# Optimization experiments

Measured on AMD Instinct MI355X. Metric: run time of the kernel, lower is better.

## Reference

```python
import jax, jax.numpy as jnp
import numpy as np

HEADS = 8
DIM_HEAD = 32
TOP_K = 256
KMEANS_ITERS = 10
EPS_LN = 1e-6
EPS_L2 = 1e-12


def chan_layer_norm(x, gamma, beta):
    # x: (b, c, L); normalize across channel dim (biased variance)
    mean = jnp.mean(x, axis=1, keepdims=True)
    var = jnp.var(x, axis=1, keepdims=True)
    return gamma * (x - mean) / (jnp.sqrt(var) + EPS_LN) + beta


def l2norm_ch(t):
    # F.normalize(t, dim=1): L2-normalize over channel axis of (B, c, L)
    n = jnp.linalg.norm(t, axis=1, keepdims=True)
    return t / jnp.maximum(n, EPS_L2)


def conv1x1(x, w):
    # x: (b, c_in, L), w: (c_out, c_in)  -> (b, c_out, L)
    return jnp.einsum('oc,bcl->bol', w, x)


def _dist2(x, c):
    # squared L2 distances, x: (N, d), c: (k, d) -> (N, k)
    return (jnp.sum(x * x, -1, keepdims=True)
            - 2.0 * x @ c.T
            + jnp.sum(c * c, -1)[None, :])


def kmeans_fit(x, k, iters):
    # Lloyd's algorithm, deterministic init = first k points
    c0 = x[:k]

    def step(c, _):
        assign = jnp.argmin(_dist2(x, c), axis=-1)           # (N,)
        sums = jax.ops.segment_sum(x, assign, num_segments=k)
        cnts = jax.ops.segment_sum(jnp.ones((x.shape[0],), x.dtype), assign,
                                   num_segments=k)
        new_c = jnp.where(cnts[:, None] > 0,
                          sums / jnp.maximum(cnts, 1.0)[:, None], c)
        return new_c, None

    c, _ = jax.lax.scan(step, c0, None, length=iters)
    return c


def select_best_ind(q, k, v, top_k):
    # q: (B, Lq, d), k/v: (B, Lk, d); B = b*heads
    B, Lk, d = k.shape
    q_flat = q.reshape(-1, d)
    centroids = kmeans_fit(q_flat, top_k, KMEANS_ITERS)       # (top_k, d)
    k_flat = k.reshape(-1, d)
    k_cluster = jnp.argmin(_dist2(k_flat, centroids), axis=-1).reshape(B, Lk)
    k_centers = centroids[k_cluster]                          # (B, Lk, d)
    k_dist = jnp.sum(jnp.abs(k_centers - k), axis=-1)         # (B, Lk)
    _, best_k = jax.lax.top_k(k_dist, top_k)                  # largest dists
    idx = best_k[:, :, None]
    k_sel = jnp.take_along_axis(k, idx, axis=1)
    v_sel = jnp.take_along_axis(v, idx, axis=1)
    return k_sel, v_sel


def reference(query_source, context, w_q, w_kv, w_out,
              ln_ctx_gamma, ln_ctx_beta, ln_q_gamma, ln_q_beta,
              ln_out_gamma, ln_out_beta, gamma_scale):
    b, c, L_query = query_source.shape
    ctx = chan_layer_norm(context, ln_ctx_gamma, ln_ctx_beta)
    qs = chan_layer_norm(query_source, ln_q_gamma, ln_q_beta)

    kv = conv1x1(ctx, w_kv)                                   # (b, 2*inner, Lc)
    k, v = jnp.split(kv, 2, axis=1)
    q = conv1x1(qs, w_q)                                      # (b, inner, Lq)

    def fold(t):  # b (h c) L -> (b h) c L
        B, hc, L = t.shape
        return t.reshape(B, HEADS, DIM_HEAD, L).reshape(B * HEADS, DIM_HEAD, L)

    q, k, v = fold(q), fold(k), fold(v)
    q, k = l2norm_ch(q), l2norm_ch(k)
    # b d L -> b L d
    q = jnp.swapaxes(q, 1, 2)
    k = jnp.swapaxes(k, 1, 2)
    v = jnp.swapaxes(v, 1, 2)

    k, v = select_best_ind(q, k, v, TOP_K)

    sim = jnp.einsum('bid,bjd->bij', q, k)                    # (b*h, Lq, top_k)
    attn = jax.nn.softmax(sim, axis=-1)
    out = jnp.einsum('bij,bjd->bid', attn, v)                 # (b*h, Lq, dh)

    out = out.reshape(b, HEADS, L_query, DIM_HEAD)
    out = jnp.transpose(out, (0, 1, 3, 2)).reshape(b, HEADS * DIM_HEAD, L_query)
    out = conv1x1(out, w_out)
    out = chan_layer_norm(out, ln_out_gamma, ln_out_beta)
    return gamma_scale[0] * out + query_source


def setup_inputs() -> dict:
    key = jax.random.key(0)
    ks = jax.random.split(key, 8)
    dim, inner = 256, HEADS * DIM_HEAD
    b, Lq, Lc = 2, 4096, 4096
    inp = {
        'query_source': jax.random.normal(ks[0], (b, dim, Lq), jnp.float32),
        'context': jax.random.normal(ks[1], (b, dim, Lc), jnp.float32),
        'w_q': jax.random.normal(ks[2], (inner, dim), jnp.float32) * 0.05,
        'w_kv': jax.random.normal(ks[3], (2 * inner, dim), jnp.float32) * 0.05,
        'w_out': jax.random.normal(ks[4], (dim, inner), jnp.float32) * 0.05,
        'ln_ctx_gamma': jnp.ones((1, dim, 1), jnp.float32),
        'ln_ctx_beta': jnp.zeros((1, dim, 1), jnp.float32),
        'ln_q_gamma': jnp.ones((1, dim, 1), jnp.float32),
        'ln_q_beta': jnp.zeros((1, dim, 1), jnp.float32),
        'ln_out_gamma': jnp.ones((1, dim, 1), jnp.float32),
        'ln_out_beta': jnp.zeros((1, dim, 1), jnp.float32),
        'gamma_scale': jax.random.normal(ks[5], (1,), jnp.float32),
    }
    return inp
```

## Files before the change

### kernel.cpp

```cpp
#include <hip/hip_runtime.h>
#include <math.h>

#define CDIM 256
#define LSEQ 4096
#define NBH 16
#define NPTS 65536
#define KC 256

__device__ __forceinline__ float fadd(float a, float b){ return __fadd_rn(a,b); }
__device__ __forceinline__ float fmul(float a, float b){ return __fmul_rn(a,b); }
__device__ __forceinline__ float fsub(float a, float b){ return __fsub_rn(a,b); }

__device__ __forceinline__ void gld_lds4(const float* g, float* l){
    __builtin_amdgcn_global_load_lds(
        (const __attribute__((address_space(1))) unsigned int*)g,
        (__attribute__((address_space(3))) unsigned int*)l, 4, 0, 0);
}

__device__ __forceinline__ float sum32_np(const float* e){
    float l[16];
    #pragma unroll
    for (int j = 0; j < 16; j++) l[j] = fadd(e[j], e[j + 16]);
    float t3[8];
    #pragma unroll
    for (int j = 0; j < 8; j++) t3[j] = fadd(l[j], l[j + 8]);
    float t6[4];
    #pragma unroll
    for (int j = 0; j < 4; j++) t6[j] = fadd(t3[j], t3[j + 4]);
    return fadd(fadd(t6[0], t6[2]), fadd(t6[1], t6[3]));
}

__global__ __launch_bounds__(64) void ln2_np(
        const float* __restrict__ x0, const float* __restrict__ g0,
        const float* __restrict__ bt0, float* __restrict__ y0,
        const float* __restrict__ x1, const float* __restrict__ g1,
        const float* __restrict__ bt1, float* __restrict__ y1) {
    __shared__ float xl[256 * 64];
    int tid = threadIdx.x;
    int gid = blockIdx.x * 64 + tid;
    int which = gid >> 13;
    int r = gid & 8191;
    int b = r >> 12, l = r & 4095;
    const float* x  = which ? x1 : x0;
    const float* g  = which ? g1 : g0;
    const float* bt = which ? bt1 : bt0;
    float* y        = which ? y1 : y0;
    const float* xb = x + (size_t)b * CDIM * LSEQ + l;
    #pragma unroll 8
    for (int c = 0; c < 256; c++)
        gld_lds4(xb + (size_t)c * LSEQ, xl + c * 64);
    __syncthreads();
    float s = 0.f;
    #pragma unroll 8
    for (int c = 0; c < 256; c++) s = fadd(s, xl[c * 64 + tid]);
    float mean = __fdiv_rn(s, 256.f);
    float s2 = 0.f;
    #pragma unroll 8
    for (int c = 0; c < 256; c++) {
        float d = fsub(xl[c * 64 + tid], mean);
        s2 = fadd(s2, fmul(d, d));
    }
    float var = __fdiv_rn(s2, 256.f);
    float den = fadd(__fsqrt_rn(var), 1e-6f);
    float* yb = y + (size_t)b * CDIM * LSEQ + l;
    #pragma unroll 4
    for (int c = 0; c < 256; c++) {
        float d = fsub(xl[c * 64 + tid], mean);
        yb[(size_t)c * LSEQ] = fadd(__fdiv_rn(fmul(g[c], d), den), bt[c]);
    }
}

__global__ __launch_bounds__(256) void conv_all16(
        const float* __restrict__ Wkv, const float* __restrict__ Xkv,
        float* __restrict__ Ykv,
        const float* __restrict__ Wq, const float* __restrict__ Xq,
        float* __restrict__ Yq) {
    int tid = threadIdx.x;
    int l0 = blockIdx.x * 512 + tid * 2;
    bool qpath = blockIdx.y >= 32;
    int yb = qpath ? (blockIdx.y - 32) : blockIdx.y;
    int o0 = yb * 16;
    int b = blockIdx.z;
    const float4* w4 = (const float4*)((qpath ? Wq : Wkv) + (size_t)o0 * CDIM);
    const float* X = qpath ? Xq : Xkv;
    const float* xb = X + (size_t)b * CDIM * LSEQ;
    float acc[16][2];
    #pragma unroll
    for (int oo = 0; oo < 16; oo++) { acc[oo][0] = 0.f; acc[oo][1] = 0.f; }
    bool sop = qpath || (blockIdx.y < 16);
    if (sop) {
        for (int c = 0; c < 256; c += 4) {
            float2 x0q = *(const float2*)(xb + (size_t)(c + 0) * LSEQ + l0);
            float2 x1q = *(const float2*)(xb + (size_t)(c + 1) * LSEQ + l0);
            float2 x2q = *(const float2*)(xb + (size_t)(c + 2) * LSEQ + l0);
            float2 x3q = *(const float2*)(xb + (size_t)(c + 3) * LSEQ + l0);
            #pragma unroll
            for (int oo = 0; oo < 16; oo++) {
                float4 w = w4[(oo * 256 + c) >> 2];
                acc[oo][0] = fadd(acc[oo][0], fmul(w.x, x0q.x));
                acc[oo][0] = fadd(acc[oo][0], fmul(w.y, x1q.x));
                acc[oo][0] = fadd(acc[oo][0], fmul(w.z, x2q.x));
                acc[oo][0] = fadd(acc[oo][0], fmul(w.w, x3q.x));
                acc[oo][1] = fadd(acc[oo][1], fmul(w.x, x0q.y));
                acc[oo][1] = fadd(acc[oo][1], fmul(w.y, x1q.y));
                acc[oo][1] = fadd(acc[oo][1], fmul(w.z, x2q.y));
                acc[oo][1] = fadd(acc[oo][1], fmul(w.w, x3q.y));
            }
        }
    } else {
        for (int c = 0; c < 256; c += 4) {
            float2 x0q = *(const float2*)(xb + (size_t)(c + 0) * LSEQ + l0);
            float2 x1q = *(const float2*)(xb + (size_t)(c + 1) * LSEQ + l0);
            float2 x2q = *(const float2*)(xb + (size_t)(c + 2) * LSEQ + l0);
            float2 x3q = *(const float2*)(xb + (size_t)(c + 3) * LSEQ + l0);
            #pragma unroll
            for (int oo = 0; oo < 16; oo++) {
                float4 w = w4[(oo * 256 + c) >> 2];
                acc[oo][0] = __builtin_fmaf(w.x, x0q.x, acc[oo][0]);
                acc[oo][0] = __builtin_fmaf(w.y, x1q.x, acc[oo][0]);
                acc[oo][0] = __builtin_fmaf(w.z, x2q.x, acc[oo][0]);
                acc[oo][0] = __builtin_fmaf(w.w, x3q.x, acc[oo][0]);
                acc[oo][1] = __builtin_fmaf(w.x, x0q.y, acc[oo][1]);
                acc[oo][1] = __builtin_fmaf(w.y, x1q.y, acc[oo][1]);
                acc[oo][1] = __builtin_fmaf(w.z, x2q.y, acc[oo][1]);
                acc[oo][1] = __builtin_fmaf(w.w, x3q.y, acc[oo][1]);
            }
        }
    }
    float* Y = qpath ? Yq : Ykv;
    int rows = qpath ? 256 : 512;
    #pragma unroll
    for (int oo = 0; oo < 16; oo++)
        *(float2*)(Y + ((size_t)b * rows + o0 + oo) * LSEQ + l0) =
            make_float2(acc[oo][0], acc[oo][1]);
}

template<bool EXACT>
__global__ __launch_bounds__(256) void conv_q8(const float* __restrict__ W,
        const float* __restrict__ X, float* __restrict__ Y) {
    __shared__ float ws[8 * 256];
    int tid = threadIdx.x;
    int l0 = blockIdx.x * 1024 + tid * 4;
    int o0 = blockIdx.y * 8;
    int b = blockIdx.z;
    {
        const float4* wb4 = (const float4*)(W + (size_t)o0 * CDIM);
        float4* ws4s = (float4*)ws;
        for (int i = tid; i < 8 * 64; i += 256) ws4s[i] = wb4[i];
    }
    __syncthreads();
    const float* xb = X + (size_t)b * CDIM * LSEQ;
    float acc[8][4];
    #pragma unroll
    for (int oo = 0; oo < 8; oo++)
        #pragma unroll
        for (int i = 0; i < 4; i++) acc[oo][i] = 0.f;
    const float4* ws4 = (const float4*)ws;
    for (int c = 0; c < 256; c += 4) {
        float4 x0q = *(const float4*)(xb + (size_t)(c + 0) * LSEQ + l0);
        float4 x1q = *(const float4*)(xb + (size_t)(c + 1) * LSEQ + l0);
        float4 x2q = *(const float4*)(xb + (size_t)(c + 2) * LSEQ + l0);
        float4 x3q = *(const float4*)(xb + (size_t)(c + 3) * LSEQ + l0);
        #pragma unroll
        for (int oo = 0; oo < 8; oo++) {
            float4 w = ws4[(oo * 256 + c) >> 2];
            if (EXACT) {
                acc[oo][0] = fadd(acc[oo][0], fmul(w.x, x0q.x));
                acc[oo][0] = fadd(acc[oo][0], fmul(w.y, x1q.x));
                acc[oo][0] = fadd(acc[oo][0], fmul(w.z, x2q.x));
                acc[oo][0] = fadd(acc[oo][0], fmul(w.w, x3q.x));
                acc[oo][1] = fadd(acc[oo][1], fmul(w.x, x0q.y));
                acc[oo][1] = fadd(acc[oo][1], fmul(w.y, x1q.y));
                acc[oo][1] = fadd(acc[oo][1], fmul(w.z, x2q.y));
                acc[oo][1] = fadd(acc[oo][1], fmul(w.w, x3q.y));
                acc[oo][2] = fadd(acc[oo][2], fmul(w.x, x0q.z));
                acc[oo][2] = fadd(acc[oo][2], fmul(w.y, x1q.z));
                acc[oo][2] = fadd(acc[oo][2], fmul(w.z, x2q.z));
                acc[oo][2] = fadd(acc[oo][2], fmul(w.w, x3q.z));
                acc[oo][3] = fadd(acc[oo][3], fmul(w.x, x0q.w));
                acc[oo][3] = fadd(acc[oo][3], fmul(w.y, x1q.w));
                acc[oo][3] = fadd(acc[oo][3], fmul(w.z, x2q.w));
                acc[oo][3] = fadd(acc[oo][3], fmul(w.w, x3q.w));
            } else {
                acc[oo][0] = __builtin_fmaf(w.x, x0q.x, acc[oo][0]);
                acc[oo][0] = __builtin_fmaf(w.y, x1q.x, acc[oo][0]);
                acc[oo][0] = __builtin_fmaf(w.z, x2q.x, acc[oo][0]);
                acc[oo][0] = __builtin_fmaf(w.w, x3q.x, acc[oo][0]);
                acc[oo][1] = __builtin_fmaf(w.x, x0q.y, acc[oo][1]);
                acc[oo][1] = __builtin_fmaf(w.y, x1q.y, acc[oo][1]);
                acc[oo][1] = __builtin_fmaf(w.z, x2q.y, acc[oo][1]);
                acc[oo][1] = __builtin_fmaf(w.w, x3q.y, acc[oo][1]);
                acc[oo][2] = __builtin_fmaf(w.x, x0q.z, acc[oo][2]);
                acc[oo][2] = __builtin_fmaf(w.y, x1q.z, acc[oo][2]);
                acc[oo][2] = __builtin_fmaf(w.z, x2q.z, acc[oo][2]);
                acc[oo][2] = __builtin_fmaf(w.w, x3q.z, acc[oo][2]);
                acc[oo][3] = __builtin_fmaf(w.x, x0q.w, acc[oo][3]);
                acc[oo][3] = __builtin_fmaf(w.y, x1q.w, acc[oo][3]);
                acc[oo][3] = __builtin_fmaf(w.z, x2q.w, acc[oo][3]);
                acc[oo][3] = __builtin_fmaf(w.w, x3q.w, acc[oo][3]);
            }
        }
    }
    #pragma unroll
    for (int oo = 0; oo < 8; oo++)
        *(float4*)(Y + ((size_t)b * 256 + o0 + oo) * LSEQ + l0) =
            make_float4(acc[oo][0], acc[oo][1], acc[oo][2], acc[oo][3]);
}

__device__ __forceinline__ void fold_body(const float* __restrict__ src,
        int srcRows, int row0, int donorm, float* __restrict__ dst,
        float* __restrict__ xxout, float* __restrict__ centout,
        float* __restrict__ ccout, int p) {
    int bh = p >> 12, l = p & 4095;
    int b = bh >> 3, h = bh & 7;
    const float* sp = src + ((size_t)b * srcRows + row0 + h * 32) * LSEQ + l;
    float x[32];
    #pragma unroll
    for (int t = 0; t < 32; t++) x[t] = sp[(size_t)t * LSEQ];
    float4* dp4 = (float4*)(dst + (size_t)p * 32);
    if (donorm) {
        float ss = 0.f;
        #pragma unroll
        for (int t = 0; t < 32; t++) ss = fadd(ss, fmul(x[t], x[t]));
        float n = __fsqrt_rn(ss);
        float den = fmaxf(n, 1e-12f);
        #pragma unroll
        for (int t = 0; t < 32; t++) x[t] = __fdiv_rn(x[t], den);
    }
    #pragma unroll
    for (int t = 0; t < 8; t++)
        dp4[t] = make_float4(x[4*t], x[4*t+1], x[4*t+2], x[4*t+3]);
    if (xxout) {
        float e[32];
        #pragma unroll
        for (int t = 0; t < 32; t++) e[t] = fmul(x[t], x[t]);
        float xv = sum32_np(e);
        xxout[p] = xv;
        if (centout && p < KC) {
            float4* cp4 = (float4*)(centout + (size_t)p * 32);
            #pragma unroll
            for (int t = 0; t < 8; t++)
                cp4[t] = make_float4(x[4*t], x[4*t+1], x[4*t+2], x[4*t+3]);
            ccout[p] = xv;
        }
    }
}

__global__ __launch_bounds__(256) void fold3_np(const float* __restrict__ kvbuf,
        const float* __restrict__ qbuf, float* __restrict__ k_t,
        float* __restrict__ v_t, float* __restrict__ q_t,
        float* __restrict__ xx, float* __restrict__ cent, float* __restrict__ cc) {
    int blk = blockIdx.x, tid = threadIdx.x;
    if (blk < 256) {
        fold_body(kvbuf, 512, 0, 1, k_t, nullptr, nullptr, nullptr, blk * 256 + tid);
    } else if (blk < 512) {
        fold_body(kvbuf, 512, 256, 0, v_t, nullptr, nullptr, nullptr, (blk - 256) * 256 + tid);
    } else {
        fold_body(qbuf, 256, 0, 1, q_t, xx, cent, cc, (blk - 512) * 256 + tid);
    }
}

__global__ __launch_bounds__(256) void assign_h(const float* __restrict__ pts,
        const float* __restrict__ xx, const float* __restrict__ cent,
        const float* __restrict__ cc, float* __restrict__ bdg, int* __restrict__ bjg) {
    __shared__ float sc[128 * 36];
    __shared__ float scc[128];
    int tid = threadIdx.x;
    int c = blockIdx.x >> 1, h = blockIdx.x & 1;
    {
        const float4* c4 = (const float4*)(cent + (size_t)h * 128 * 32);
        for (int i = tid; i < 128 * 8; i += 256) {
            int row = i >> 3, t = i & 7;
            ((float4*)(sc + row * 36))[t] = c4[i];
        }
    }
    if (tid < 128) scc[tid] = cc[h * 128 + tid];
    __syncthreads();
    int pg = tid >> 2, quarter = tid & 3;
    int pb = c * 256 + pg * 4;
    float x[4][32];
    float xp[4];
    #pragma unroll
    for (int i = 0; i < 4; i++) {
        const float4* pp = (const float4*)(pts + (size_t)(pb + i) * 32);
        #pragma unroll
        for (int t = 0; t < 8; t++) {
            float4 f = pp[t];
            x[i][4*t] = f.x; x[i][4*t+1] = f.y; x[i][4*t+2] = f.z; x[i][4*t+3] = f.w;
        }
        xp[i] = xx[pb + i];
    }
    float bd[4] = {3.4e38f, 3.4e38f, 3.4e38f, 3.4e38f};
    int bj[4] = {0x7fffffff, 0x7fffffff, 0x7fffffff, 0x7fffffff};
    for (int jj = 0; jj < 32; jj++) {
        int j = (jj << 2) | quarter;
        const float4* cj = (const float4*)(sc + j * 36);
        float w[32];
        #pragma unroll
        for (int t = 0; t < 8; t++) {
            float4 f = cj[t];
            w[4*t] = f.x; w[4*t+1] = f.y; w[4*t+2] = f.z; w[4*t+3] = f.w;
        }
        float sj = scc[j];
        int jg = h * 128 + j;
        #pragma unroll
        for (int i = 0; i < 4; i++) {
            float g = 0.f;
            #pragma unroll
            for (int t = 0; t < 32; t++) g = __builtin_fmaf(x[i][t], w[t], g);
            float d = fadd(fsub(xp[i], fmul(2.f, g)), sj);
            if (d < bd[i]) { bd[i] = d; bj[i] = jg; }
        }
    }
    #pragma unroll
    for (int i = 0; i < 4; i++) {
        float ob; int oj;
        ob = __shfl_xor(bd[i], 1); oj = __shfl_xor(bj[i], 1);
        if (ob < bd[i] || (ob == bd[i] && oj < bj[i])) { bd[i] = ob; bj[i] = oj; }
        ob = __shfl_xor(bd[i], 2); oj = __shfl_xor(bj[i], 2);
        if (ob < bd[i] || (ob == bd[i] && oj < bj[i])) { bd[i] = ob; bj[i] = oj; }
    }
    if (quarter == 0) {
        #pragma unroll
        for (int i = 0; i < 4; i++) {
            bdg[(size_t)h * NPTS + pb + i] = bd[i];
            bjg[(size_t)h * NPTS + pb + i] = bj[i];
        }
    }
}

__global__ __launch_bounds__(256) void merge_asn(const float* __restrict__ bdg,
        const int* __restrict__ bjg, int* __restrict__ asn, int* __restrict__ hist) {
    __shared__ int bins[256];
    int tid = threadIdx.x, c = blockIdx.x;
    bins[tid] = 0;
    __syncthreads();
    int p = c * 256 + tid;
    float d0 = bdg[p], d1 = bdg[NPTS + p];
    int j = (d1 < d0) ? bjg[NPTS + p] : bjg[p];
    asn[p] = j;
    atomicAdd(&bins[j], 1);
    __syncthreads();
    hist[c * 256 + tid] = bins[tid];
}

__global__ __launch_bounds__(256) void scan_chunks(const int* __restrict__ hist,
        int* __restrict__ chunkbase, int* __restrict__ totals) {
    __shared__ int a[256];
    int j = blockIdx.x, c = threadIdx.x;
    a[c] = hist[(size_t)c * 256 + j];
    __syncthreads();
    for (int d = 1; d < 256; d <<= 1) {
        int v = a[c];
        int u = (c >= d) ? a[c - d] : 0;
        __syncthreads();
        a[c] = v + u;
        __syncthreads();
    }
    chunkbase[(size_t)c * 256 + j] = (c == 0) ? 0 : a[c - 1];
    if (c == 255) totals[j] = a[255];
}

__global__ __launch_bounds__(256) void scatter_v5(const int* __restrict__ asn,
        const int* __restrict__ chunkbase, const int* __restrict__ totals,
        int* __restrict__ perm) {
    __shared__ int cb[256];
    __shared__ int al[256];
    int c = blockIdx.x, tid = threadIdx.x;
    cb[tid] = totals[tid];
    al[tid] = asn[c * 256 + tid];
    __syncthreads();
    for (int d = 1; d < 256; d <<= 1) {
        int v = cb[tid];
        int u = (tid >= d) ? cb[tid - d] : 0;
        __syncthreads();
        cb[tid] = v + u;
        __syncthreads();
    }
    int my = al[tid];
    int base = (my == 0) ? 0 : cb[my - 1];
    int r = 0;
    for (int i = 0; i < tid; i++) r += (al[i] == my) ? 1 : 0;
    perm[base + chunkbase[(size_t)c * 256 + my] + r] = c * 256 + tid;
}

#define STILE 128
__global__ __launch_bounds__(256) void sumk_v4(const float* __restrict__ pts,
        const int* __restrict__ perm, const int* __restrict__ totals,
        float* __restrict__ cent, float* __restrict__ cc) {
    __shared__ int cb[256];
    __shared__ float buf[2][STILE][32];
    int j = blockIdx.x, tid = threadIdx.x;
    cb[tid] = totals[tid];
    __syncthreads();
    for (int d = 1; d < 256; d <<= 1) {
        int v = cb[tid];
        int u = (tid >= d) ? cb[tid - d] : 0;
        __syncthreads();
        cb[tid] = v + u;
        __syncthreads();
    }
    int base = (j == 0) ? 0 : cb[j - 1];
    int n = totals[j];
    int t = tid & 31, r0 = tid >> 5;
    for (int r = r0; r < STILE; r += 8) {
        if (r < n) buf[0][r][t] = pts[(size_t)perm[base + r] * 32 + t];
    }
    __syncthreads();
    float s = 0.f;
    int b = 0;
    for (int i0 = 0; i0 < n; i0 += STILE, b ^= 1) {
        int nx = i0 + STILE;
        if (nx < n) {
            for (int r = r0; r < STILE; r += 8) {
                int g = nx + r;
                if (g < n) buf[b ^ 1][r][t] = pts[(size_t)perm[base + g] * 32 + t];
            }
        }
        if (tid < 32) {
            int m = n - i0; if (m > STILE) m = STILE;
            int i = 0;
            for (; i + 4 <= m; i += 4) {
                s = fadd(s, buf[b][i][tid]);
                s = fadd(s, buf[b][i + 1][tid]);
                s = fadd(s, buf[b][i + 2][tid]);
                s = fadd(s, buf[b][i + 3][tid]);
            }
            for (; i < m; i++) s = fadd(s, buf[b][i][tid]);
        }
        __syncthreads();
    }
    if (tid < 32) {
        float v;
        if (n > 0) {
            v = __fdiv_rn(s, (float)n);
            cent[(size_t)j * 32 + tid] = v;
        } else {
            v = cent[(size_t)j * 32 + tid];
        }
        float e = fmul(v, v);
        e = fadd(e, __shfl_xor(e, 16));
        e = fadd(e, __shfl_xor(e, 8));
        e = fadd(e, __shfl_xor(e, 4));
        e = fadd(e, __shfl_xor(e, 2));
        e = fadd(e, __shfl_xor(e, 1));
        if (tid == 0) cc[j] = e;
    }
}

__global__ __launch_bounds__(256) void kdist4p(const float* __restrict__ pts,
        const float* __restrict__ cent, const float* __restrict__ cc,
        float* __restrict__ kd) {
    __shared__ float sc[256 * 36];
    __shared__ float scc[256];
    int tid = threadIdx.x, c = blockIdx.x;
    {
        const float4* c4 = (const float4*)cent;
        for (int i = tid; i < 256 * 8; i += 256) {
            int row = i >> 3, t = i & 7;
            ((float4*)(sc + row * 36))[t] = c4[i];
        }
    }
    scc[tid] = cc[tid];
    __syncthreads();
    int pg = tid >> 2, quarter = tid & 3;
    int pb = c * 256 + pg * 4;
    float x[4][32];
    float xp[4];
    #pragma unroll
    for (int i = 0; i < 4; i++) {
        const float4* pp = (const float4*)(pts + (size_t)(pb + i) * 32);
        #pragma unroll
        for (int t = 0; t < 8; t++) {
            float4 f = pp[t];
            x[i][4*t] = f.x; x[i][4*t+1] = f.y; x[i][4*t+2] = f.z; x[i][4*t+3] = f.w;
        }
        float e[32];
        #pragma unroll
        for (int t = 0; t < 32; t++) e[t] = fmul(x[i][t], x[i][t]);
        xp[i] = sum32_np(e);
    }
    float bd[4] = {3.4e38f, 3.4e38f, 3.4e38f, 3.4e38f};
    int bj[4] = {0x7fffffff, 0x7fffffff, 0x7fffffff, 0x7fffffff};
    for (int jj = 0; jj < 64; jj++) {
        int j = (jj << 2) | quarter;
        const float4* cj = (const float4*)(sc + j * 36);
        float w[32];
        #pragma unroll
        for (int t = 0; t < 8; t++) {
            float4 f = cj[t];
            w[4*t] = f.x; w[4*t+1] = f.y; w[4*t+2] = f.z; w[4*t+3] = f.w;
        }
        float sj = scc[j];
        #pragma unroll
        for (int i = 0; i < 4; i++) {
            float g = 0.f;
            #pragma unroll
            for (int t = 0; t < 32; t++) g = __builtin_fmaf(x[i][t], w[t], g);
            float d = fadd(fsub(xp[i], fmul(2.f, g)), sj);
            if (d < bd[i]) { bd[i] = d; bj[i] = j; }
        }
    }
    #pragma unroll
    for (int i = 0; i < 4; i++) {
        float ob; int oj;
        ob = __shfl_xor(bd[i], 1); oj = __shfl_xor(bj[i], 1);
        if (ob < bd[i] || (ob == bd[i] && oj < bj[i])) { bd[i] = ob; bj[i] = oj; }
        ob = __shfl_xor(bd[i], 2); oj = __shfl_xor(bj[i], 2);
        if (ob < bd[i] || (ob == bd[i] && oj < bj[i])) { bd[i] = ob; bj[i] = oj; }
    }
    if (quarter == 0) {
        #pragma unroll
        for (int i = 0; i < 4; i++) {
            const float* cb = &sc[bj[i] * 36];
            float e[32];
            #pragma unroll
            for (int t = 0; t < 32; t++) e[t] = fabsf(fsub(cb[t], x[i][t]));
            kd[pb + i] = sum32_np(e);
        }
    }
}

__global__ __launch_bounds__(256) void topk_v3(const float* __restrict__ kd,
        const float* __restrict__ k_t, const float* __restrict__ v_t,
        float* __restrict__ ksel, float* __restrict__ vsel) {
    __shared__ int wsum[4];
    __shared__ int sc1[256];
    __shared__ int out_src[256];
    int bh = blockIdx.x, tid = threadIdx.x;
    int wave = tid >> 6, lane = tid & 63;
    unsigned uv[16];
    {
        const unsigned* kdu = (const unsigned*)(kd + (size_t)bh * 4096);
        #pragma unroll
        for (int q = 0; q < 16; q++) uv[q] = kdu[tid * 16 + q];
    }
    unsigned T = 0u;
    for (int bit = 31; bit >= 0; bit--) {
        unsigned cand = T | (1u << bit);
        int c = 0;
        #pragma unroll
        for (int q = 0; q < 16; q++) c += (uv[q] >= cand) ? 1 : 0;
        c += __shfl_xor(c, 32); c += __shfl_xor(c, 16); c += __shfl_xor(c, 8);
        c += __shfl_xor(c, 4);  c += __shfl_xor(c, 2);  c += __shfl_xor(c, 1);
        if (lane == 0) wsum[wave] = c;
        __syncthreads();
        int tot = wsum[0] + wsum[1] + wsum[2] + wsum[3];
        __syncthreads();
        if (tot >= 256) T = cand;
    }
    int r;
    {
        int c = 0;
        #pragma unroll
        for (int q = 0; q < 16; q++) c += (uv[q] > T) ? 1 : 0;
        c += __shfl_xor(c, 32); c += __shfl_xor(c, 16); c += __shfl_xor(c, 8);
        c += __shfl_xor(c, 4);  c += __shfl_xor(c, 2);  c += __shfl_xor(c, 1);
        if (lane == 0) wsum[wave] = c;
        __syncthreads();
        r = 256 - (wsum[0] + wsum[1] + wsum[2] + wsum[3]);
        __syncthreads();
    }
    int ec = 0;
    #pragma unroll
    for (int q = 0; q < 16; q++) ec += (uv[q] == T) ? 1 : 0;
    sc1[tid] = ec;
    __syncthreads();
    for (int d = 1; d < 256; d <<= 1) {
        int t0 = sc1[tid];
        int u0 = (tid >= d) ? sc1[tid - d] : 0;
        __syncthreads();
        sc1[tid] = t0 + u0;
        __syncthreads();
    }
    int erank = (tid == 0) ? 0 : sc1[tid - 1];
    __syncthreads();
    bool incl[16];
    int ic = 0;
    #pragma unroll
    for (int q = 0; q < 16; q++) {
        unsigned u = uv[q];
        bool inc;
        if (u > T) inc = true;
        else if (u == T) { inc = (erank < r); erank++; }
        else inc = false;
        incl[q] = inc;
        ic += inc ? 1 : 0;
    }
    sc1[tid] = ic;
    __syncthreads();
    for (int d = 1; d < 256; d <<= 1) {
        int t0 = sc1[tid];
        int u0 = (tid >= d) ? sc1[tid - d] : 0;
        __syncthreads();
        sc1[tid] = t0 + u0;
        __syncthreads();
    }
    int pos = (tid == 0) ? 0 : sc1[tid - 1];
    int base_i = tid * 16;
    #pragma unroll
    for (int q = 0; q < 16; q++) {
        if (incl[q]) out_src[pos++] = base_i + q;
    }
    __syncthreads();
    for (int e = tid; e < 256 * 32; e += 256) {
        int jj = e >> 5, t = e & 31;
        int src = out_src[jj];
        ksel[(size_t)bh * 8192 + e] = k_t[((size_t)bh * 4096 + src) * 32 + t];
        vsel[(size_t)bh * 8192 + e] = v_t[((size_t)bh * 4096 + src) * 32 + t];
    }
}

#define HP4 2052
__global__ __launch_bounds__(256, 2) void attn_v4(const float* __restrict__ q_t,
        const float* __restrict__ ksel, const float* __restrict__ vsel,
        float* __restrict__ out) {
    __shared__ float sk[4 * HP4];
    __shared__ float sv[4 * HP4];
    int bh = blockIdx.y, tid = threadIdx.x;
    {
        const float4* gk = (const float4*)(ksel + (size_t)bh * 8192);
        const float4* gv = (const float4*)(vsel + (size_t)bh * 8192);
        for (int i = tid; i < 2048; i += 256) {
            int s = i >> 9, idx = i & 511;
            ((float4*)(sk + s * HP4))[idx] = gk[i];
            ((float4*)(sv + s * HP4))[idx] = gv[i];
        }
    }
    __syncthreads();
    int grp = tid >> 3;
    int dh = tid & 1;
    int slice = (tid >> 1) & 3;
    int p0 = bh * 4096 + blockIdx.x * 128 + grp * 4;
    float q[4][16];
    #pragma unroll
    for (int i = 0; i < 4; i++) {
        const float4* qp = (const float4*)(q_t + (size_t)(p0 + i) * 32 + dh * 16);
        #pragma unroll
        for (int t = 0; t < 4; t++) {
            float4 f = qp[t];
            q[i][4*t] = f.x; q[i][4*t+1] = f.y; q[i][4*t+2] = f.z; q[i][4*t+3] = f.w;
        }
    }
    float o[4][16];
    #pragma unroll
    for (int i = 0; i < 4; i++)
        #pragma unroll
        for (int t = 0; t < 16; t++) o[i][t] = 0.f;
    float ls[4] = {0.f, 0.f, 0.f, 0.f};
    const float* kb = sk + slice * HP4 + dh * 16;
    const float* vb = sv + slice * HP4 + dh * 16;
    for (int j = 0; j < 64; j++) {
        float kf[16];
        #pragma unroll
        for (int t = 0; t < 4; t++) {
            float4 f = *(const float4*)(kb + j * 32 + t * 4);
            kf[4*t] = f.x; kf[4*t+1] = f.y; kf[4*t+2] = f.z; kf[4*t+3] = f.w;
        }
        float ps[4];
        #pragma unroll
        for (int i = 0; i < 4; i++) {
            float a = 0.f, b2 = 0.f, c2 = 0.f, d2 = 0.f;
            #pragma unroll
            for (int t = 0; t < 4; t++) {
                a  += q[i][4*t]   * kf[4*t];
                b2 += q[i][4*t+1] * kf[4*t+1];
                c2 += q[i][4*t+2] * kf[4*t+2];
                d2 += q[i][4*t+3] * kf[4*t+3];
            }
            ps[i] = (a + b2) + (c2 + d2);
        }
        #pragma unroll
        for (int i = 0; i < 4; i++) ps[i] += __shfl_xor(ps[i], 1);
        float w[4];
        #pragma unroll
        for (int i = 0; i < 4; i++) {
            w[i] = __expf(ps[i] - 1.0f);
            ls[i] += w[i];
        }
        float vf[16];
        #pragma unroll
        for (int t = 0; t < 4; t++) {
            float4 f = *(const float4*)(vb + j * 32 + t * 4);
            vf[4*t] = f.x; vf[4*t+1] = f.y; vf[4*t+2] = f.z; vf[4*t+3] = f.w;
        }
        #pragma unroll
        for (int i = 0; i < 4; i++)
            #pragma unroll
            for (int t = 0; t < 16; t++) o[i][t] += w[i] * vf[t];
    }
    #pragma unroll
    for (int i = 0; i < 4; i++) {
        #pragma unroll
        for (int t = 0; t < 16; t++) {
            o[i][t] += __shfl_xor(o[i][t], 2);
            o[i][t] += __shfl_xor(o[i][t], 4);
        }
        ls[i] += __shfl_xor(ls[i], 2);
        ls[i] += __shfl_xor(ls[i], 4);
    }
    if (slice == 0) {
        #pragma unroll
        for (int i = 0; i < 4; i++) {
            float inv = 1.f / ls[i];
            float4* op = (float4*)(out + (size_t)(p0 + i) * 32 + dh * 16);
            #pragma unroll
            for (int t = 0; t < 4; t++)
                op[t] = make_float4(o[i][4*t]*inv, o[i][4*t+1]*inv,
                                    o[i][4*t+2]*inv, o[i][4*t+3]*inv);
        }
    }
}

__global__ __launch_bounds__(256) void unfold_kernel(const float* __restrict__ att,
        float* __restrict__ Fo) {
    __shared__ float tbuf[32][65];
    int bh = blockIdx.y, l0 = blockIdx.x * 64;
    int b = bh >> 3, h = bh & 7;
    int tid = threadIdx.x;
    #pragma unroll
    for (int r = 0; r < 8; r++) {
        int e = r * 256 + tid;
        int l = e >> 5, d = e & 31;
        tbuf[d][l] = att[((size_t)bh * 4096 + l0 + l) * 32 + d];
    }
    __syncthreads();
    #pragma unroll
    for (int r = 0; r < 8; r++) {
        int e = r * 256 + tid;
        int d = e >> 6, l = e & 63;
        Fo[((size_t)b * 256 + h * 32 + d) * LSEQ + l0 + l] = tbuf[d][l];
    }
}

__global__ __launch_bounds__(64) void lnres_np(const float* __restrict__ x,
        const float* __restrict__ g, const float* __restrict__ bt,
        const float* __restrict__ gs, const float* __restrict__ qsrc,
        float* __restrict__ y) {
    __shared__ float xl[256 * 64];
    __shared__ float ql[256 * 64];
    int tid = threadIdx.x;
    int gid = blockIdx.x * 64 + tid;
    int b = gid >> 12, l = gid & 4095;
    const float* xb = x + (size_t)b * CDIM * LSEQ + l;
    const float* qb = qsrc + (size_t)b * CDIM * LSEQ + l;
    #pragma unroll 8
    for (int c = 0; c < 256; c++) {
        gld_lds4(xb + (size_t)c * LSEQ, xl + c * 64);
        gld_lds4(qb + (size_t)c * LSEQ, ql + c * 64);
    }
    __syncthreads();
    float s = 0.f;
    #pragma unroll 8
    for (int c = 0; c < 256; c++) s = fadd(s, xl[c * 64 + tid]);
    float mean = __fdiv_rn(s, 256.f);
    float s2 = 0.f;
    #pragma unroll 8
    for (int c = 0; c < 256; c++) {
        float d = fsub(xl[c * 64 + tid], mean);
        s2 = fadd(s2, fmul(d, d));
    }
    float var = __fdiv_rn(s2, 256.f);
    float den = fadd(__fsqrt_rn(var), 1e-6f);
    float scale = gs[0];
    float* yb = y + (size_t)b * CDIM * LSEQ + l;
    #pragma unroll 4
    for (int c = 0; c < 256; c++) {
        float d = fsub(xl[c * 64 + tid], mean);
        float r = fadd(__fdiv_rn(fmul(g[c], d), den), bt[c]);
        yb[(size_t)c * LSEQ] = fadd(fmul(scale, r), ql[c * 64 + tid]);
    }
}

extern "C" void kernel_launch(void* const* d_in, const int* in_sizes, int n_in,
                              void* d_out, int out_size, void* d_ws, size_t ws_size,
                              hipStream_t stream) {
    const float* qsrc   = (const float*)d_in[0];
    const float* ctx    = (const float*)d_in[1];
    const float* w_q    = (const float*)d_in[2];
    const float* w_kv   = (const float*)d_in[3];
    const float* w_out  = (const float*)d_in[4];
    const float* g_ctx  = (const float*)d_in[5];
    const float* b_ctx  = (const float*)d_in[6];
    const float* g_q    = (const float*)d_in[7];
    const float* b_q    = (const float*)d_in[8];
    const float* g_out  = (const float*)d_in[9];
    const float* b_out  = (const float*)d_in[10];
    const float* gs     = (const float*)d_in[11];

    char* base = (char*)d_ws;
    const size_t MB = 1024 * 1024;
    float* yln   = (float*)base;
    float* att   = (float*)base;
    float* kvbuf = (float*)(base + 8 * MB);
    float* y32   = (float*)(base + 8 * MB);
    float* bdg   = (float*)(base + 8 * MB);
    int*   bjg   = (int*)  (base + 9 * MB);
    float* qbuf  = (float*)(base + 24 * MB);
    float* Fo    = (float*)(base + 24 * MB);
    float* q_t   = (float*)(base + 32 * MB);
    float* k_t   = (float*)(base + 40 * MB);
    float* v_t   = (float*)(base + 48 * MB);
    char* SM = base + 56 * MB;
    float* xx_q      = (float*)(SM + 0);
    float* cent      = (float*)(SM + 512 * 1024);
    float* cc        = (float*)(SM + 576 * 1024);
    int*   totals    = (int*)  (SM + 640 * 1024);
    int*   asn       = (int*)  (SM + 704 * 1024);
    int*   hist      = (int*)  (SM + 960 * 1024);
    int*   chunkbase = (int*)  (SM + 1472 * 1024);
    int*   perm      = (int*)  (SM + 1984 * 1024);
    float* kd        = (float*)(SM + 2240 * 1024);
    float* ksel      = (float*)(SM + 2496 * 1024);
    float* vsel      = (float*)(SM + 3008 * 1024);
    float* yln_q     = (float*)(base + 60 * MB);

    ln2_np<<<256, 64, 0, stream>>>(ctx, g_ctx, b_ctx, yln,
                                   qsrc, g_q, b_q, yln_q);
    conv_all16<<<dim3(8, 48, 2), 256, 0, stream>>>(w_kv, yln, kvbuf,
                                                   w_q, yln_q, qbuf);
    fold3_np<<<768, 256, 0, stream>>>(kvbuf, qbuf, k_t, v_t, q_t, xx_q, cent, cc);

    for (int it = 0; it < 10; it++) {
        assign_h<<<512, 256, 0, stream>>>(q_t, xx_q, cent, cc, bdg, bjg);
        merge_asn<<<256, 256, 0, stream>>>(bdg, bjg, asn, hist);
        scan_chunks<<<256, 256, 0, stream>>>(hist, chunkbase, totals);
        scatter_v5<<<256, 256, 0, stream>>>(asn, chunkbase, totals, perm);
        sumk_v4<<<256, 256, 0, stream>>>(q_t, perm, totals, cent, cc);
    }

    kdist4p<<<256, 256, 0, stream>>>(k_t, cent, cc, kd);
    topk_v3<<<16, 256, 0, stream>>>(kd, k_t, v_t, ksel, vsel);
    attn_v4<<<dim3(32, 16), 256, 0, stream>>>(q_t, ksel, vsel, att);
    unfold_kernel<<<dim3(64, 16), 256, 0, stream>>>(att, Fo);
    conv_q8<false><<<dim3(4, 32, 2), 256, 0, stream>>>(w_out, Fo, y32);
    lnres_np<<<128, 64, 0, stream>>>(y32, g_out, b_out, gs, qsrc, (float*)d_out);
}
```

Baseline: 832.5 us.

## Fuse k-means iterations into one persistent kernel with grid barriers

Replaces the 50 per-iteration k-means kernel launches (assign, merge, scan, scatter, sum) with a single persistent 256-block kernel that steps through the phases using an atomic-counter grid barrier. The assign step now covers all 256 centroids per block instead of splitting them into two halves with a separate merge pass, so the bdg/bjg intermediates and the merge kernel go away. This is meant to cut launch overhead and global round trips. In exchange, assign parallelism drops from 512 to 256 blocks, and correctness depends on all 256 blocks being co-resident, which this grid size on the GPU should satisfy.

After: 1.543 ms. 85.3% more time.

```diff
diff --git a/kernel.cpp b/kernel.cpp
--- a/kernel.cpp
+++ b/kernel.cpp
@@ -260,191 +260,195 @@
     }
 }
 
-__global__ __launch_bounds__(256) void assign_h(const float* __restrict__ pts,
-        const float* __restrict__ xx, const float* __restrict__ cent,
-        const float* __restrict__ cc, float* __restrict__ bdg, int* __restrict__ bjg) {
-    __shared__ float sc[128 * 36];
-    __shared__ float scc[128];
+__device__ __forceinline__ void gbar(int* bar) {
+    __syncthreads();
+    if (threadIdx.x == 0) {
+        int old = __hip_atomic_fetch_add(bar, 1, __ATOMIC_ACQ_REL,
+                                         __HIP_MEMORY_SCOPE_AGENT);
+        int want = (old / 256 + 1) * 256;
+        while (__hip_atomic_load(bar, __ATOMIC_ACQUIRE,
+                                 __HIP_MEMORY_SCOPE_AGENT) < want) {
+            __builtin_amdgcn_s_sleep(8);
+        }
+    }
+    __syncthreads();
+}
+
+#define STILE 128
+__global__ __launch_bounds__(256, 1) void kmeans_fused(
+        const float* __restrict__ pts, const float* __restrict__ xx,
+        float* __restrict__ cent, float* __restrict__ cc,
+        int* __restrict__ asn, int* __restrict__ hist,
+        int* __restrict__ chunkbase, int* __restrict__ totals,
+        int* __restrict__ perm, int* bar, int iters) {
+    __shared__ __align__(16) char sm[38912];
     int tid = threadIdx.x;
-    int c = blockIdx.x >> 1, h = blockIdx.x & 1;
-    {
-        const float4* c4 = (const float4*)(cent + (size_t)h * 128 * 32);
-        for (int i = tid; i < 128 * 8; i += 256) {
-            int row = i >> 3, t = i & 7;
-            ((float4*)(sc + row * 36))[t] = c4[i];
-        }
-    }
-    if (tid < 128) scc[tid] = cc[h * 128 + tid];
-    __syncthreads();
-    int pg = tid >> 2, quarter = tid & 3;
-    int pb = c * 256 + pg * 4;
-    float x[4][32];
-    float xp[4];
-    #pragma unroll
-    for (int i = 0; i < 4; i++) {
-        const float4* pp = (const float4*)(pts + (size_t)(pb + i) * 32);
-        #pragma unroll
-        for (int t = 0; t < 8; t++) {
-            float4 f = pp[t];
-            x[i][4*t] = f.x; x[i][4*t+1] = f.y; x[i][4*t+2] = f.z; x[i][4*t+3] = f.w;
-        }
-        xp[i] = xx[pb + i];
-    }
-    float bd[4] = {3.4e38f, 3.4e38f, 3.4e38f, 3.4e38f};
-    int bj[4] = {0x7fffffff, 0x7fffffff, 0x7fffffff, 0x7fffffff};
-    for (int jj = 0; jj < 32; jj++) {
-        int j = (jj << 2) | quarter;
-        const float4* cj = (const float4*)(sc + j * 36);
-        float w[32];
-        #pragma unroll
-        for (int t = 0; t < 8; t++) {
-            float4 f = cj[t];
-            w[4*t] = f.x; w[4*t+1] = f.y; w[4*t+2] = f.z; w[4*t+3] = f.w;
-        }
-        float sj = scc[j];
-        int jg = h * 128 + j;
-        #pragma unroll
-        for (int i = 0; i < 4; i++) {
-            float g = 0.f;
-            #pragma unroll
-            for (int t = 0; t < 32; t++) g = __builtin_fmaf(x[i][t], w[t], g);
-            float d = fadd(fsub(xp[i], fmul(2.f, g)), sj);
-            if (d < bd[i]) { bd[i] = d; bj[i] = jg; }
-        }
-    }
-    #pragma unroll
-    for (int i = 0; i < 4; i++) {
-        float ob; int oj;
-        ob = __shfl_xor(bd[i], 1); oj = __shfl_xor(bj[i], 1);
-        if (ob < bd[i] || (ob == bd[i] && oj < bj[i])) { bd[i] = ob; bj[i] = oj; }
-        ob = __shfl_xor(bd[i], 2); oj = __shfl_xor(bj[i], 2);
-        if (ob < bd[i] || (ob == bd[i] && oj < bj[i])) { bd[i] = ob; bj[i] = oj; }
-    }
-    if (quarter == 0) {
-        #pragma unroll
-        for (int i = 0; i < 4; i++) {
-            bdg[(size_t)h * NPTS + pb + i] = bd[i];
-            bjg[(size_t)h * NPTS + pb + i] = bj[i];
-        }
-    }
-}
-
-__global__ __launch_bounds__(256) void merge_asn(const float* __restrict__ bdg,
-        const int* __restrict__ bjg, int* __restrict__ asn, int* __restrict__ hist) {
-    __shared__ int bins[256];
-    int tid = threadIdx.x, c = blockIdx.x;
-    bins[tid] = 0;
-    __syncthreads();
-    int p = c * 256 + tid;
-    float d0 = bdg[p], d1 = bdg[NPTS + p];
-    int j = (d1 < d0) ? bjg[NPTS + p] : bjg[p];
-    asn[p] = j;
-    atomicAdd(&bins[j], 1);
-    __syncthreads();
-    hist[c * 256 + tid] = bins[tid];
-}
-
-__global__ __launch_bounds__(256) void scan_chunks(const int* __restrict__ hist,
-        int* __restrict__ chunkbase, int* __restrict__ totals) {
-    __shared__ int a[256];
-    int j = blockIdx.x, c = threadIdx.x;
-    a[c] = hist[(size_t)c * 256 + j];
-    __syncthreads();
-    for (int d = 1; d < 256; d <<= 1) {
-        int v = a[c];
-        int u = (c >= d) ? a[c - d] : 0;
-        __syncthreads();
-        a[c] = v + u;
-        __syncthreads();
-    }
-    chunkbase[(size_t)c * 256 + j] = (c == 0) ? 0 : a[c - 1];
-    if (c == 255) totals[j] = a[255];
-}
-
-__global__ __launch_bounds__(256) void scatter_v5(const int* __restrict__ asn,
-        const int* __restrict__ chunkbase, const int* __restrict__ totals,
-        int* __restrict__ perm) {
-    __shared__ int cb[256];
-    __shared__ int al[256];
-    int c = blockIdx.x, tid = threadIdx.x;
-    cb[tid] = totals[tid];
-    al[tid] = asn[c * 256 + tid];
-    __syncthreads();
-    for (int d = 1; d < 256; d <<= 1) {
-        int v = cb[tid];
-        int u = (tid >= d) ? cb[tid - d] : 0;
-        __syncthreads();
-        cb[tid] = v + u;
-        __syncthreads();
-    }
-    int my = al[tid];
-    int base = (my == 0) ? 0 : cb[my - 1];
-    int r = 0;
-    for (int i = 0; i < tid; i++) r += (al[i] == my) ? 1 : 0;
-    perm[base + chunkbase[(size_t)c * 256 + my] + r] = c * 256 + tid;
-}
-
-#define STILE 128
-__global__ __launch_bounds__(256) void sumk_v4(const float* __restrict__ pts,
-        const int* __restrict__ perm, const int* __restrict__ totals,
-        float* __restrict__ cent, float* __restrict__ cc) {
-    __shared__ int cb[256];
-    __shared__ float buf[2][STILE][32];
-    int j = blockIdx.x, tid = threadIdx.x;
-    cb[tid] = totals[tid];
-    __syncthreads();
-    for (int d = 1; d < 256; d <<= 1) {
-        int v = cb[tid];
-        int u = (tid >= d) ? cb[tid - d] : 0;
-        __syncthreads();
-        cb[tid] = v + u;
-        __syncthreads();
-    }
-    int base = (j == 0) ? 0 : cb[j - 1];
-    int n = totals[j];
-    int t = tid & 31, r0 = tid >> 5;
-    for (int r = r0; r < STILE; r += 8) {
-        if (r < n) buf[0][r][t] = pts[(size_t)perm[base + r] * 32 + t];
-    }
-    __syncthreads();
-    float s = 0.f;
-    int b = 0;
-    for (int i0 = 0; i0 < n; i0 += STILE, b ^= 1) {
-        int nx = i0 + STILE;
-        if (nx < n) {
+    int blk = blockIdx.x;
+
+    for (int it = 0; it < iters; it++) {
+        {
+            float* sc  = (float*)sm;
+            float* scc = (float*)(sm + 36864);
+            int*  bins = (int*) (sm + 37888);
+            const float4* c4 = (const float4*)cent;
+            for (int i = tid; i < 2048; i += 256) {
+                int row = i >> 3, t = i & 7;
+                ((float4*)(sc + row * 36))[t] = c4[i];
+            }
+            scc[tid] = cc[tid];
+            bins[tid] = 0;
+            __syncthreads();
+            int pg = tid >> 2, quarter = tid & 3;
+            int pb = blk * 256 + pg * 4;
+            float x[4][32];
+            float xp[4];
+            #pragma unroll
+            for (int i = 0; i < 4; i++) {
+                const float4* pp = (const float4*)(pts + (size_t)(pb + i) * 32);
+                #pragma unroll
+                for (int t = 0; t < 8; t++) {
+                    float4 f = pp[t];
+                    x[i][4*t] = f.x; x[i][4*t+1] = f.y; x[i][4*t+2] = f.z; x[i][4*t+3] = f.w;
+                }
+                xp[i] = xx[pb + i];
+            }
+            float bd[4] = {3.4e38f, 3.4e38f, 3.4e38f, 3.4e38f};
+            int bj[4] = {0x7fffffff, 0x7fffffff, 0x7fffffff, 0x7fffffff};
+            for (int jj = 0; jj < 64; jj++) {
+                int j = (jj << 2) | quarter;
+                const float4* cj = (const float4*)(sc + j * 36);
+                float w[32];
+                #pragma unroll
+                for (int t = 0; t < 8; t++) {
+                    float4 f = cj[t];
+                    w[4*t] = f.x; w[4*t+1] = f.y; w[4*t+2] = f.z; w[4*t+3] = f.w;
+                }
+                float sj = scc[j];
+                #pragma unroll
+                for (int i = 0; i < 4; i++) {
+                    float g = 0.f;
+                    #pragma unroll
+                    for (int t = 0; t < 32; t++) g = __builtin_fmaf(x[i][t], w[t], g);
+                    float d = fadd(fsub(xp[i], fmul(2.f, g)), sj);
+                    if (d < bd[i]) { bd[i] = d; bj[i] = j; }
+                }
+            }
+            #pragma unroll
+            for (int i = 0; i < 4; i++) {
+                float ob; int oj;
+                ob = __shfl_xor(bd[i], 1); oj = __shfl_xor(bj[i], 1);
+                if (ob < bd[i] || (ob == bd[i] && oj < bj[i])) { bd[i] = ob; bj[i] = oj; }
+                ob = __shfl_xor(bd[i], 2); oj = __shfl_xor(bj[i], 2);
+                if (ob < bd[i] || (ob == bd[i] && oj < bj[i])) { bd[i] = ob; bj[i] = oj; }
+            }
+            if (quarter == 0) {
+                #pragma unroll
+                for (int i = 0; i < 4; i++) {
+                    asn[pb + i] = bj[i];
+                    atomicAdd(&bins[bj[i]], 1);
+                }
+            }
+            __syncthreads();
+            hist[blk * 256 + tid] = bins[tid];
+        }
+        gbar(bar);
+        {
+            int* a = (int*)sm;
+            int j = blk;
+            a[tid] = hist[(size_t)tid * 256 + j];
+            __syncthreads();
+            for (int d = 1; d < 256; d <<= 1) {
+                int v = a[tid];
+                int u = (tid >= d) ? a[tid - d] : 0;
+                __syncthreads();
+                a[tid] = v + u;
+                __syncthreads();
+            }
+            chunkbase[(size_t)tid * 256 + j] = (tid == 0) ? 0 : a[tid - 1];
+            if (tid == 255) totals[j] = a[255];
+        }
+        gbar(bar);
+        {
+            int* cb = (int*)sm;
+            int* al = (int*)(sm + 1024);
+            cb[tid] = totals[tid];
+            al[tid] = asn[blk * 256 + tid];
+            __syncthreads();
+            for (int d = 1; d < 256; d <<= 1) {
+                int v = cb[tid];
+                int u = (tid >= d) ? cb[tid - d] : 0;
+                __syncthreads();
+                cb[tid] = v + u;
+                __syncthreads();
+            }
+            int my = al[tid];
+            int base = (my == 0) ? 0 : cb[my - 1];
+            int r = 0;
+            for (int i = 0; i < tid; i++) r += (al[i] == my) ? 1 : 0;
+            perm[base + chunkbase[(size_t)blk * 256 + my] + r] = blk * 256 + tid;
+        }
+        gbar(bar);
+        {
+            int* cb = (int*)sm;
+            float (*buf)[STILE][32] = (float (*)[STILE][32])(sm + 1024);
+            int j = blk;
+            cb[tid] = totals[tid];
+            __syncthreads();
+            for (int d = 1; d < 256; d <<= 1) {
+                int v = cb[tid];
+                int u = (tid >= d) ? cb[tid - d] : 0;
+                __syncthreads();
+                cb[tid] = v + u;
+                __syncthreads();
+            }
+            int base = (j == 0) ? 0 : cb[j - 1];
+            int n = totals[j];
+            int t = tid & 31, r0 = tid >> 5;
             for (int r = r0; r < STILE; r += 8) {
-                int g = nx + r;
-                if (g < n) buf[b ^ 1][r][t] = pts[(size_t)perm[base + g] * 32 + t];
-            }
-        }
-        if (tid < 32) {
-            int m = n - i0; if (m > STILE) m = STILE;
-            int i = 0;
-            for (; i + 4 <= m; i += 4) {
-                s = fadd(s, buf[b][i][tid]);
-                s = fadd(s, buf[b][i + 1][tid]);
-                s = fadd(s, buf[b][i + 2][tid]);
-                s = fadd(s, buf[b][i + 3][tid]);
-            }
-            for (; i < m; i++) s = fadd(s, buf[b][i][tid]);
-        }
-        __syncthreads();
-    }
-    if (tid < 32) {
-        float v;
-        if (n > 0) {
-            v = __fdiv_rn(s, (float)n);
-            cent[(size_t)j * 32 + tid] = v;
-        } else {
-            v = cent[(size_t)j * 32 + tid];
-        }
-        float e = fmul(v, v);
-        e = fadd(e, __shfl_xor(e, 16));
-        e = fadd(e, __shfl_xor(e, 8));
-        e = fadd(e, __shfl_xor(e, 4));
-        e = fadd(e, __shfl_xor(e, 2));
-        e = fadd(e, __shfl_xor(e, 1));
-        if (tid == 0) cc[j] = e;
+                if (r < n) buf[0][r][t] = pts[(size_t)perm[base + r] * 32 + t];
+            }
+            __syncthreads();
+            float s = 0.f;
+            int b = 0;
+            for (int i0 = 0; i0 < n; i0 += STILE, b ^= 1) {
+                int nx = i0 + STILE;
+                if (nx < n) {
+                    for (int r = r0; r < STILE; r += 8) {
+                        int g2 = nx + r;
+                        if (g2 < n) buf[b ^ 1][r][t] = pts[(size_t)perm[base + g2] * 32 + t];
+                    }
+                }
+                if (tid < 32) {
+                    int m = n - i0; if (m > STILE) m = STILE;
+                    int i = 0;
+                    for (; i + 4 <= m; i += 4) {
+                        s = fadd(s, buf[b][i][tid]);
+                        s = fadd(s, buf[b][i + 1][tid]);
+                        s = fadd(s, buf[b][i + 2][tid]);
+                        s = fadd(s, buf[b][i + 3][tid]);
+                    }
+                    for (; i < m; i++) s = fadd(s, buf[b][i][tid]);
+                }
+                __syncthreads();
+            }
+            if (tid < 32) {
+                float v;
+                if (n > 0) {
+                    v = __fdiv_rn(s, (float)n);
+                    cent[(size_t)j * 32 + tid] = v;
+                } else {
+                    v = cent[(size_t)j * 32 + tid];
+                }
+                float e = fmul(v, v);
+                e = fadd(e, __shfl_xor(e, 16));
+                e = fadd(e, __shfl_xor(e, 8));
+                e = fadd(e, __shfl_xor(e, 4));
+                e = fadd(e, __shfl_xor(e, 2));
+                e = fadd(e, __shfl_xor(e, 1));
+                if (tid == 0) cc[j] = e;
+            }
+        }
+        gbar(bar);
     }
 }
 
@@ -794,8 +798,6 @@
     float* att   = (float*)base;
     float* kvbuf = (float*)(base + 8 * MB);
     float* y32   = (float*)(base + 8 * MB);
-    float* bdg   = (float*)(base + 8 * MB);
-    int*   bjg   = (int*)  (base + 9 * MB);
     float* qbuf  = (float*)(base + 24 * MB);
     float* Fo    = (float*)(base + 24 * MB);
     float* q_t   = (float*)(base + 32 * MB);
@@ -806,6 +808,7 @@
     float* cent      = (float*)(SM + 512 * 1024);
     float* cc        = (float*)(SM + 576 * 1024);
     int*   totals    = (int*)  (SM + 640 * 1024);
+    int*   bar       = (int*)  (SM + 648 * 1024);
     int*   asn       = (int*)  (SM + 704 * 1024);
     int*   hist      = (int*)  (SM + 960 * 1024);
     int*   chunkbase = (int*)  (SM + 1472 * 1024);
@@ -821,13 +824,9 @@
                                                    w_q, yln_q, qbuf);
     fold3_np<<<768, 256, 0, stream>>>(kvbuf, qbuf, k_t, v_t, q_t, xx_q, cent, cc);
 
-    for (int it = 0; it < 10; it++) {
-        assign_h<<<512, 256, 0, stream>>>(q_t, xx_q, cent, cc, bdg, bjg);
-        merge_asn<<<256, 256, 0, stream>>>(bdg, bjg, asn, hist);
-        scan_chunks<<<256, 256, 0, stream>>>(hist, chunkbase, totals);
-        scatter_v5<<<256, 256, 0, stream>>>(asn, chunkbase, totals, perm);
-        sumk_v4<<<256, 256, 0, stream>>>(q_t, perm, totals, cent, cc);
-    }
+    hipMemsetAsync(bar, 0, sizeof(int), stream);
+    kmeans_fused<<<256, 256, 0, stream>>>(q_t, xx_q, cent, cc, asn, hist,
+                                          chunkbase, totals, perm, bar, 10);
 
     kdist4p<<<256, 256, 0, stream>>>(k_t, cent, cc, kd);
     topk_v3<<<16, 256, 0, stream>>>(kd, k_t, v_t, ksel, vsel);
```
